# Kernel tuning notes

Hardware: AMD Instinct MI355X
Metric: run time of the kernel (lower is better)

The kernel has to match this reference:

```python
import jax, jax.numpy as jnp
import numpy as np

D_IN = 512
EMBED = 256
N = 8192

def setup_inputs() -> dict:
    key = jax.random.key(0)
    ks = jax.random.split(key, 6)
    s_in = 1.0 / np.sqrt(D_IN)
    s_e = 1.0 / np.sqrt(EMBED)
    return {
        "X": jax.random.normal(ks[0], (N, D_IN), dtype=jnp.float32),
        "W_Q": jax.random.uniform(ks[1], (EMBED, D_IN), jnp.float32, -s_in, s_in),
        "W_K": jax.random.uniform(ks[2], (EMBED, D_IN), jnp.float32, -s_in, s_in),
        "W_V": jax.random.uniform(ks[3], (EMBED, D_IN), jnp.float32, -s_in, s_in),
        "head_w": jax.random.uniform(ks[4], (1, EMBED), jnp.float32, -s_e, s_e),
        "head_b": jax.random.uniform(ks[5], (1,), jnp.float32, -s_e, s_e),
    }

def reference(X, W_Q, W_K, W_V, head_w, head_b):
    # Projections: nn.Linear(x) = x @ W.T
    Q = X @ W_Q.T                      # [N, D]
    K = X @ W_K.T                      # [N, D]
    V = X @ W_V.T                      # [N, D]
    A = Q @ K.T                        # [N, N] unnormalized linear attention
    Z = A @ V                          # [N, D]
    preds = Z @ head_w.T + head_b      # [N, 1]
    return preds[:, 0]                 # [N]
```

## Files before the change

### kernel.cpp

```cpp
#include <hip/hip_runtime.h>

#define D_IN 512
#define EMBED 256
#define NBLK1 256
#define SCALE 16777216.0f
#define INV_SCALE 5.9604644775390625e-08f

#define WS_WVP_B 0
#define WS_TFX_B 8192
#define WS_RFX_B 40960
#define N_ZERO   6144

typedef unsigned long long ull;

__global__ __launch_bounds__(64) void k_wv(const float* __restrict__ W_V,
                                           const float* __restrict__ head_w,
                                           float* __restrict__ wvp,
                                           ull* __restrict__ zbase) {
    const int cg  = blockIdx.x & 7;
    const int eg  = blockIdx.x >> 3;
    const int col = cg * 64 + threadIdx.x;
    float acc = 0.f;
    const int e0 = eg * 64;
#pragma unroll 8
    for (int e = e0; e < e0 + 64; ++e) acc += head_w[e] * W_V[(size_t)e * D_IN + col];
    wvp[(size_t)eg * D_IN + col] = acc;

    const int g = blockIdx.x * 64 + threadIdx.x;
    for (int i = g; i < N_ZERO; i += 32 * 64) zbase[i] = 0ull;
}

__global__ __launch_bounds__(512) void k_pass1(const float* __restrict__ X,
                                               const float* __restrict__ wvp,
                                               ull* __restrict__ t_fixed) {
    const int tid  = threadIdx.x;
    const int lane = tid & 63;
    const int wid  = tid >> 6;
    const int c0   = lane * 4;
    const int c1   = 256 + lane * 4;

    float4 wv0 = {0.f,0.f,0.f,0.f}, wv1 = {0.f,0.f,0.f,0.f};
#pragma unroll
    for (int eg = 0; eg < 4; ++eg) {
        const float4 a = *(const float4*)(wvp + (size_t)eg * D_IN + c0);
        const float4 b = *(const float4*)(wvp + (size_t)eg * D_IN + c1);
        wv0.x += a.x; wv0.y += a.y; wv0.z += a.z; wv0.w += a.w;
        wv1.x += b.x; wv1.y += b.y; wv1.z += b.z; wv1.w += b.w;
    }

    float4 t0 = {0.f,0.f,0.f,0.f};
    float4 t1 = {0.f,0.f,0.f,0.f};

    const int row0 = blockIdx.x * 32 + wid * 4;
#pragma unroll
    for (int r = 0; r < 4; ++r) {
        const float* xr = X + (size_t)(row0 + r) * D_IN;
        const float4 a = *(const float4*)(xr + c0);
        const float4 b = *(const float4*)(xr + c1);
        float p = a.x * wv0.x + a.y * wv0.y + a.z * wv0.z + a.w * wv0.w
                + b.x * wv1.x + b.y * wv1.y + b.z * wv1.z + b.w * wv1.w;
#pragma unroll
        for (int off = 32; off >= 1; off >>= 1) p += __shfl_xor(p, off, 64);
        t0.x += p * a.x; t0.y += p * a.y; t0.z += p * a.z; t0.w += p * a.w;
        t1.x += p * b.x; t1.y += p * b.y; t1.z += p * b.z; t1.w += p * b.w;
    }

    __shared__ float lds[8][D_IN];
    *(float4*)(&lds[wid][c0]) = t0;
    *(float4*)(&lds[wid][c1]) = t1;
    __syncthreads();

    float s = 0.f;
#pragma unroll
    for (int w = 0; w < 8; ++w) s += lds[w][tid];
    const long long v = llrintf(s * SCALE);
    atomicAdd(&t_fixed[(size_t)(blockIdx.x & 7) * D_IN + tid], (ull)v);
}

__global__ __launch_bounds__(512) void k_ur(const ull* __restrict__ t_fixed,
                                            const float* __restrict__ W_K,
                                            const float* __restrict__ W_Q,
                                            ull* __restrict__ r_fixed) {
    __shared__ float t_lds[D_IN];
    const int tid = threadIdx.x;

    long long acc = 0;
#pragma unroll
    for (int j = 0; j < 8; ++j) acc += (long long)t_fixed[(size_t)j * D_IN + tid];
    t_lds[tid] = (float)acc * INV_SCALE;
    __syncthreads();

    const int lane = tid & 63;
    const int w    = tid >> 6;
    const int e    = blockIdx.x * 8 + w;
    const int c0   = lane * 4;
    const int c1   = 256 + lane * 4;

    const float4 ta = *(const float4*)(t_lds + c0);
    const float4 tb = *(const float4*)(t_lds + c1);
    const float4 ka = *(const float4*)(W_K + (size_t)e * D_IN + c0);
    const float4 kb = *(const float4*)(W_K + (size_t)e * D_IN + c1);
    float p = ta.x * ka.x + ta.y * ka.y + ta.z * ka.z + ta.w * ka.w
            + tb.x * kb.x + tb.y * kb.y + tb.z * kb.z + tb.w * kb.w;
#pragma unroll
    for (int off = 32; off >= 1; off >>= 1) p += __shfl_xor(p, off, 64);

    const float4 qa = *(const float4*)(W_Q + (size_t)e * D_IN + c0);
    const float4 qb = *(const float4*)(W_Q + (size_t)e * D_IN + c1);
    ull* rr = r_fixed + (size_t)(blockIdx.x & 3) * D_IN;
    atomicAdd(&rr[c0 + 0], (ull)(long long)llrintf(p * qa.x * SCALE));
    atomicAdd(&rr[c0 + 1], (ull)(long long)llrintf(p * qa.y * SCALE));
    atomicAdd(&rr[c0 + 2], (ull)(long long)llrintf(p * qa.z * SCALE));
    atomicAdd(&rr[c0 + 3], (ull)(long long)llrintf(p * qa.w * SCALE));
    atomicAdd(&rr[c1 + 0], (ull)(long long)llrintf(p * qb.x * SCALE));
    atomicAdd(&rr[c1 + 1], (ull)(long long)llrintf(p * qb.y * SCALE));
    atomicAdd(&rr[c1 + 2], (ull)(long long)llrintf(p * qb.z * SCALE));
    atomicAdd(&rr[c1 + 3], (ull)(long long)llrintf(p * qb.w * SCALE));
}

__global__ __launch_bounds__(512) void k_pass2(const float* __restrict__ X,
                                               const ull* __restrict__ r_fixed,
                                               const float* __restrict__ head_b,
                                               float* __restrict__ out) {
    __shared__ float r_lds[D_IN];
    const int tid = threadIdx.x;

    long long acc = 0;
#pragma unroll
    for (int j = 0; j < 4; ++j) acc += (long long)r_fixed[(size_t)j * D_IN + tid];
    r_lds[tid] = (float)acc * INV_SCALE;
    __syncthreads();

    const int lane = tid & 63;
    const int wid  = tid >> 6;
    const int c0   = lane * 4;
    const int c1   = 256 + lane * 4;

    const float4 r0 = *(const float4*)(r_lds + c0);
    const float4 r1 = *(const float4*)(r_lds + c1);
    const float bb  = head_b[0];

    const int row0 = blockIdx.x * 32 + wid * 4;
#pragma unroll
    for (int rr = 0; rr < 4; ++rr) {
        const int row = row0 + rr;
        const float* xr = X + (size_t)row * D_IN;
        const float4 a = *(const float4*)(xr + c0);
        const float4 b = *(const float4*)(xr + c1);
        float p = a.x * r0.x + a.y * r0.y + a.z * r0.z + a.w * r0.w
                + b.x * r1.x + b.y * r1.y + b.z * r1.z + b.w * r1.w;
#pragma unroll
        for (int off = 32; off >= 1; off >>= 1) p += __shfl_xor(p, off, 64);
        if (lane == 0) out[row] = p + bb;
    }
}

extern "C" void kernel_launch(void* const* d_in, const int* in_sizes, int n_in,
                              void* d_out, int out_size, void* d_ws, size_t ws_size,
                              hipStream_t stream) {
    const float* X      = (const float*)d_in[0];
    const float* W_Q    = (const float*)d_in[1];
    const float* W_K    = (const float*)d_in[2];
    const float* W_V    = (const float*)d_in[3];
    const float* head_w = (const float*)d_in[4];
    const float* head_b = (const float*)d_in[5];
    float* out = (float*)d_out;

    char* ws = (char*)d_ws;
    float* wvp    = (float*)(ws + WS_WVP_B);
    ull*   t_fix  = (ull*)  (ws + WS_TFX_B);
    ull*   r_fix  = (ull*)  (ws + WS_RFX_B);

    k_wv   <<<32,    64, 0, stream>>>(W_V, head_w, wvp, t_fix);
    k_pass1<<<NBLK1, 512, 0, stream>>>(X, wvp, t_fix);
    k_ur   <<<32,   512, 0, stream>>>(t_fix, W_K, W_Q, r_fix);
    k_pass2<<<NBLK1, 512, 0, stream>>>(X, r_fix, head_b, out);
}
```

Baseline: 26.39 us.

## Fuse pass1 and U/R stage via last-arriver grid counter, drop r atomics

Merges the k_ur kernel into k_pass1. Each block takes an arrival ticket from a global counter, and the last 32 blocks to arrive spin until all 256 have added their contributions. Those blocks then compute the W_K/W_Q stage and write per-block partial r vectors, which k_pass2 sums in plain float instead of reading fixed-point atomics. This removes one kernel launch and the many 64-bit atomic adds on r. In exchange it adds a spin-wait that relies on those 32 blocks being co-resident, plus a serial 32-way sum in pass2.

```diff
diff --git a/kernel.cpp b/kernel.cpp
--- a/kernel.cpp
+++ b/kernel.cpp
@@ -2,16 +2,17 @@
 
 #define D_IN 512
 #define EMBED 256
-#define NBLK1 256
+#define NBLK 256
 #define SCALE 16777216.0f
 #define INV_SCALE 5.9604644775390625e-08f
 
+typedef unsigned long long ull;
+
 #define WS_WVP_B 0
 #define WS_TFX_B 8192
-#define WS_RFX_B 40960
-#define N_ZERO   6144
-
-typedef unsigned long long ull;
+#define WS_CNT_B 40960
+#define WS_RP_B  45056
+#define N_ZERO   4097
 
 __global__ __launch_bounds__(64) void k_wv(const float* __restrict__ W_V,
                                            const float* __restrict__ head_w,
@@ -30,14 +31,23 @@
     for (int i = g; i < N_ZERO; i += 32 * 64) zbase[i] = 0ull;
 }
 
-__global__ __launch_bounds__(512) void k_pass1(const float* __restrict__ X,
-                                               const float* __restrict__ wvp,
-                                               ull* __restrict__ t_fixed) {
+__global__ __launch_bounds__(512) void k_pass1ur(const float* __restrict__ X,
+                                                 const float* __restrict__ wvp,
+                                                 const float* __restrict__ W_K,
+                                                 const float* __restrict__ W_Q,
+                                                 ull* __restrict__ t_fixed,
+                                                 ull* __restrict__ counter,
+                                                 float* __restrict__ rp) {
     const int tid  = threadIdx.x;
     const int lane = tid & 63;
     const int wid  = tid >> 6;
     const int c0   = lane * 4;
     const int c1   = 256 + lane * 4;
+
+    __shared__ float lds[8][D_IN];
+    __shared__ float t_lds[D_IN];
+    __shared__ float u_lds[8];
+    __shared__ unsigned arrival_s;
 
     float4 wv0 = {0.f,0.f,0.f,0.f}, wv1 = {0.f,0.f,0.f,0.f};
 #pragma unroll
@@ -50,85 +60,88 @@
 
     float4 t0 = {0.f,0.f,0.f,0.f};
     float4 t1 = {0.f,0.f,0.f,0.f};
-
     const int row0 = blockIdx.x * 32 + wid * 4;
 #pragma unroll
     for (int r = 0; r < 4; ++r) {
         const float* xr = X + (size_t)(row0 + r) * D_IN;
         const float4 a = *(const float4*)(xr + c0);
         const float4 b = *(const float4*)(xr + c1);
-        float p = a.x * wv0.x + a.y * wv0.y + a.z * wv0.z + a.w * wv0.w
-                + b.x * wv1.x + b.y * wv1.y + b.z * wv1.z + b.w * wv1.w;
+        float p = a.x*wv0.x + a.y*wv0.y + a.z*wv0.z + a.w*wv0.w
+                + b.x*wv1.x + b.y*wv1.y + b.z*wv1.z + b.w*wv1.w;
 #pragma unroll
         for (int off = 32; off >= 1; off >>= 1) p += __shfl_xor(p, off, 64);
-        t0.x += p * a.x; t0.y += p * a.y; t0.z += p * a.z; t0.w += p * a.w;
-        t1.x += p * b.x; t1.y += p * b.y; t1.z += p * b.z; t1.w += p * b.w;
+        t0.x += p*a.x; t0.y += p*a.y; t0.z += p*a.z; t0.w += p*a.w;
+        t1.x += p*b.x; t1.y += p*b.y; t1.z += p*b.z; t1.w += p*b.w;
     }
-
-    __shared__ float lds[8][D_IN];
     *(float4*)(&lds[wid][c0]) = t0;
     *(float4*)(&lds[wid][c1]) = t1;
     __syncthreads();
 
-    float s = 0.f;
+    {
+        float s = 0.f;
 #pragma unroll
-    for (int w = 0; w < 8; ++w) s += lds[w][tid];
-    const long long v = llrintf(s * SCALE);
-    atomicAdd(&t_fixed[(size_t)(blockIdx.x & 7) * D_IN + tid], (ull)v);
-}
-
-__global__ __launch_bounds__(512) void k_ur(const ull* __restrict__ t_fixed,
-                                            const float* __restrict__ W_K,
-                                            const float* __restrict__ W_Q,
-                                            ull* __restrict__ r_fixed) {
-    __shared__ float t_lds[D_IN];
-    const int tid = threadIdx.x;
-
-    long long acc = 0;
-#pragma unroll
-    for (int j = 0; j < 8; ++j) acc += (long long)t_fixed[(size_t)j * D_IN + tid];
-    t_lds[tid] = (float)acc * INV_SCALE;
+        for (int w = 0; w < 8; ++w) s += lds[w][tid];
+        const long long v = llrintf(s * SCALE);
+        ull old = atomicAdd(&t_fixed[(size_t)(blockIdx.x & 7) * D_IN + tid], (ull)v);
+        unsigned keep = (unsigned)old ^ (unsigned)(old >> 32);
+        asm volatile("" :: "v"(keep));
+    }
     __syncthreads();
 
-    const int lane = tid & 63;
-    const int w    = tid >> 6;
-    const int e    = blockIdx.x * 8 + w;
-    const int c0   = lane * 4;
-    const int c1   = 256 + lane * 4;
+    if (tid == 0) arrival_s = (unsigned)atomicAdd(counter, 1ull);
+    __syncthreads();
+    const unsigned arrival = arrival_s;
+    if (arrival < 224u) return;
+    const int k = (int)arrival - 224;
 
-    const float4 ta = *(const float4*)(t_lds + c0);
-    const float4 tb = *(const float4*)(t_lds + c1);
-    const float4 ka = *(const float4*)(W_K + (size_t)e * D_IN + c0);
-    const float4 kb = *(const float4*)(W_K + (size_t)e * D_IN + c1);
-    float p = ta.x * ka.x + ta.y * ka.y + ta.z * ka.z + ta.w * ka.w
-            + tb.x * kb.x + tb.y * kb.y + tb.z * kb.z + tb.w * kb.w;
+    if (tid == 0) {
+        while (atomicAdd(counter, 0ull) < 256ull) __builtin_amdgcn_s_sleep(8);
+    }
+    __syncthreads();
+
+    {
+        long long acc = 0;
 #pragma unroll
-    for (int off = 32; off >= 1; off >>= 1) p += __shfl_xor(p, off, 64);
+        for (int j = 0; j < 8; ++j)
+            acc += (long long)atomicAdd(&t_fixed[(size_t)j * D_IN + tid], 0ull);
+        t_lds[tid] = (float)acc * INV_SCALE;
+    }
+    __syncthreads();
 
-    const float4 qa = *(const float4*)(W_Q + (size_t)e * D_IN + c0);
-    const float4 qb = *(const float4*)(W_Q + (size_t)e * D_IN + c1);
-    ull* rr = r_fixed + (size_t)(blockIdx.x & 3) * D_IN;
-    atomicAdd(&rr[c0 + 0], (ull)(long long)llrintf(p * qa.x * SCALE));
-    atomicAdd(&rr[c0 + 1], (ull)(long long)llrintf(p * qa.y * SCALE));
-    atomicAdd(&rr[c0 + 2], (ull)(long long)llrintf(p * qa.z * SCALE));
-    atomicAdd(&rr[c0 + 3], (ull)(long long)llrintf(p * qa.w * SCALE));
-    atomicAdd(&rr[c1 + 0], (ull)(long long)llrintf(p * qb.x * SCALE));
-    atomicAdd(&rr[c1 + 1], (ull)(long long)llrintf(p * qb.y * SCALE));
-    atomicAdd(&rr[c1 + 2], (ull)(long long)llrintf(p * qb.z * SCALE));
-    atomicAdd(&rr[c1 + 3], (ull)(long long)llrintf(p * qb.w * SCALE));
+    {
+        const int e = 8 * k + wid;
+        const float4 ta = *(const float4*)(t_lds + c0);
+        const float4 tb = *(const float4*)(t_lds + c1);
+        const float4 ka = *(const float4*)(W_K + (size_t)e * D_IN + c0);
+        const float4 kb = *(const float4*)(W_K + (size_t)e * D_IN + c1);
+        float p = ta.x*ka.x + ta.y*ka.y + ta.z*ka.z + ta.w*ka.w
+                + tb.x*kb.x + tb.y*kb.y + tb.z*kb.z + tb.w*kb.w;
+#pragma unroll
+        for (int off = 32; off >= 1; off >>= 1) p += __shfl_xor(p, off, 64);
+        if (lane == 0) u_lds[wid] = p;
+    }
+    __syncthreads();
+
+    {
+        float racc = 0.f;
+#pragma unroll
+        for (int m = 0; m < 8; ++m)
+            racc += u_lds[m] * W_Q[(size_t)(8 * k + m) * D_IN + tid];
+        rp[(size_t)k * D_IN + tid] = racc;
+    }
 }
 
 __global__ __launch_bounds__(512) void k_pass2(const float* __restrict__ X,
-                                               const ull* __restrict__ r_fixed,
+                                               const float* __restrict__ rp,
                                                const float* __restrict__ head_b,
                                                float* __restrict__ out) {
     __shared__ float r_lds[D_IN];
     const int tid = threadIdx.x;
 
-    long long acc = 0;
-#pragma unroll
-    for (int j = 0; j < 4; ++j) acc += (long long)r_fixed[(size_t)j * D_IN + tid];
-    r_lds[tid] = (float)acc * INV_SCALE;
+    float acc = 0.f;
+#pragma unroll 8
+    for (int j = 0; j < 32; ++j) acc += rp[(size_t)j * D_IN + tid];
+    r_lds[tid] = acc;
     __syncthreads();
 
     const int lane = tid & 63;
@@ -147,8 +160,8 @@
         const float* xr = X + (size_t)row * D_IN;
         const float4 a = *(const float4*)(xr + c0);
         const float4 b = *(const float4*)(xr + c1);
-        float p = a.x * r0.x + a.y * r0.y + a.z * r0.z + a.w * r0.w
-                + b.x * r1.x + b.y * r1.y + b.z * r1.z + b.w * r1.w;
+        float p = a.x*r0.x + a.y*r0.y + a.z*r0.z + a.w*r0.w
+                + b.x*r1.x + b.y*r1.y + b.z*r1.z + b.w*r1.w;
 #pragma unroll
         for (int off = 32; off >= 1; off >>= 1) p += __shfl_xor(p, off, 64);
         if (lane == 0) out[row] = p + bb;
@@ -167,12 +180,12 @@
     float* out = (float*)d_out;
 
     char* ws = (char*)d_ws;
-    float* wvp    = (float*)(ws + WS_WVP_B);
-    ull*   t_fix  = (ull*)  (ws + WS_TFX_B);
-    ull*   r_fix  = (ull*)  (ws + WS_RFX_B);
+    float* wvp   = (float*)(ws + WS_WVP_B);
+    ull*   t_fix = (ull*)  (ws + WS_TFX_B);
+    ull*   cnt   = (ull*)  (ws + WS_CNT_B);
+    float* rp    = (float*)(ws + WS_RP_B);
 
-    k_wv   <<<32,    64, 0, stream>>>(W_V, head_w, wvp, t_fix);
-    k_pass1<<<NBLK1, 512, 0, stream>>>(X, wvp, t_fix);
-    k_ur   <<<32,   512, 0, stream>>>(t_fix, W_K, W_Q, r_fix);
-    k_pass2<<<NBLK1, 512, 0, stream>>>(X, r_fix, head_b, out);
+    k_wv     <<<32,   64,  0, stream>>>(W_V, head_w, wvp, t_fix);
+    k_pass1ur<<<NBLK, 512, 0, stream>>>(X, wvp, W_K, W_Q, t_fix, cnt, rp);
+    k_pass2  <<<NBLK, 512, 0, stream>>>(X, rp, head_b, out);
 }
```

New measurement: 24.63 us. 1.07x faster.
